# Kernel tuning notes

Hardware: AMD Instinct MI355X
Metric: run time of the kernel (lower is better)

The kernel has to match this reference:

```python
import jax, jax.numpy as jnp
import numpy as np

N = 50000
E = 800000
IO = 128
HID = 256
KQ = 256
EPS = 1e-5


def setup_inputs() -> dict:
    key = jax.random.key(0)
    ks = jax.random.split(key, 16)
    def w(k, shape, fan_in):
        return jax.random.normal(k, shape, dtype=jnp.float32) / np.sqrt(fan_in)
    x0 = jax.random.normal(ks[0], (N, IO), dtype=jnp.float32)
    edges = jax.random.randint(ks[1], (2, E), 0, N, dtype=jnp.int64)
    return {
        "x0": x0,
        "edges": edges,
        "Wq1": w(ks[2], (IO, KQ), IO), "Wk1": w(ks[3], (IO, KQ), IO),
        "Wv1": w(ks[4], (IO, HID), IO), "Wr1": w(ks[5], (IO, HID), IO),
        "b1": jnp.zeros((HID,), jnp.float32),
        "g1": jnp.ones((HID,), jnp.float32), "be1": jnp.zeros((HID,), jnp.float32),
        "Wq2": w(ks[6], (HID, KQ), HID), "Wk2": w(ks[7], (HID, KQ), HID),
        "Wv2": w(ks[8], (HID, IO), HID), "Wr2": w(ks[9], (HID, IO), HID),
        "b2": jnp.zeros((IO,), jnp.float32),
        "g2": jnp.ones((IO,), jnp.float32), "be2": jnp.zeros((IO,), jnp.float32),
    }


def _transformer_conv(x, src, dst, Wq, Wk, Wv, Wr, b, n):
    # single-head graph transformer conv (PyG TransformerConv style)
    q = x @ Wq                      # [n, kq]
    k = x @ Wk                      # [n, kq]
    v = x @ Wv                      # [n, out]
    scale = 1.0 / np.sqrt(Wq.shape[1])
    logits = jnp.sum(q[dst] * k[src], axis=-1) * scale   # [E]
    m = jax.lax.stop_gradient(jax.ops.segment_max(logits, dst, num_segments=n))
    m = jnp.where(jnp.isfinite(m), m, 0.0)
    e = jnp.exp(logits - m[dst])                          # [E]
    s = jax.ops.segment_sum(e, dst, num_segments=n)       # [n]
    alpha = e / jnp.maximum(s[dst], 1e-16)                # [E]
    agg = jax.ops.segment_sum(alpha[:, None] * v[src], dst, num_segments=n)
    return agg + x @ Wr + b


def _batch_norm(x, gamma, beta):
    mu = jnp.mean(x, axis=0)
    var = jnp.mean((x - mu) ** 2, axis=0)  # biased var, as torch BN training
    return (x - mu) * jax.lax.rsqrt(var + EPS) * gamma + beta


def reference(x0, edges, Wq1, Wk1, Wv1, Wr1, b1, g1, be1,
              Wq2, Wk2, Wv2, Wr2, b2, g2, be2):
    src, dst = edges[0], edges[1]
    n = x0.shape[0]
    x = _transformer_conv(x0, src, dst, Wq1, Wk1, Wv1, Wr1, b1, n)
    x = jax.nn.relu(_batch_norm(x, g1, be1))
    x = _transformer_conv(x, src, dst, Wq2, Wk2, Wv2, Wr2, b2, n)
    x = _batch_norm(x, g2, be2)
    return jax.nn.relu(x + x0)
```

## Files before the change

kernel.cpp:

```cpp
#include <hip/hip_runtime.h>
#include <stdint.h>

typedef unsigned short ushort_t;

__device__ __forceinline__ float bf2f(unsigned short u) {
  union { unsigned int i; float f; } c; c.i = ((unsigned int)u) << 16; return c.f;
}
__device__ __forceinline__ unsigned short f2bf(float f) {
  union { float f; unsigned int i; } c; c.f = f;
  unsigned int r = c.i + 0x7FFFu + ((c.i >> 16) & 1u);
  return (unsigned short)(r >> 16);
}
__device__ __forceinline__ float relu_nanprop(float v) { return (v < 0.f) ? 0.f : v; }

__device__ __forceinline__ void async_copy16(const void* g, void* l) {
  __builtin_amdgcn_global_load_lds(
      (const __attribute__((address_space(1))) unsigned int*)(uintptr_t)g,
      (__attribute__((address_space(3))) unsigned int*)(uintptr_t)l,
      16, 0, 0);
}

typedef __attribute__((ext_vector_type(8))) short s16x8;
typedef __attribute__((ext_vector_type(4))) float f32x4;

__device__ __forceinline__ int edge_at(const void* edges, int wide, int idx) {
  if (wide) return (int)((const long long*)edges)[idx];
  return ((const int*)edges)[idx];
}

__global__ void setup_kernel(int* __restrict__ zreg2, int N,
                             const int* __restrict__ e32, int n32, int* __restrict__ eflag,
                             const unsigned int* __restrict__ x, int nw, int* __restrict__ fF) {
  int b = blockIdx.x, tid = threadIdx.x;
  if (b < 256) {
    int total = 2 * N + 1024;
    for (int i = b * 256 + tid; i < total; i += 256 * 256) zreg2[i] = 0;
  } else if (b == 256) {
    __shared__ int any;
    if (tid == 0) any = 0;
    __syncthreads();
    for (int i = tid; i < 4096; i += 256) {
      int idx = 2 * i + 1;
      if (idx < n32 && e32[idx] != 0) any = 1;
    }
    __syncthreads();
    if (tid == 0) eflag[0] = (any == 0) ? 1 : 0;
  } else {
    __shared__ int cnt;
    if (tid == 0) cnt = 0;
    __syncthreads();
    int local = 0;
    for (int i = tid; i < 4096 && i < nw; i += 256) {
      unsigned int low = x[i] & 0xFFFFu;
      unsigned int e = (low >> 7) & 0xFFu;
      if (low != 0u && (e < 96u || e > 144u)) local++;
    }
    atomicAdd(&cnt, local);
    __syncthreads();
    if (tid == 0) fF[0] = (cnt > 1024) ? 1 : 0;
  }
}

__global__ void cvt_all_kernel(const void* __restrict__ x0, ushort_t* __restrict__ x0b, int nx,
                               const void* p0, const void* p1, const void* p2,
                               const void* p3, const void* p4, const void* p5,
                               ushort_t* o0, ushort_t* o1, ushort_t* o2,
                               ushort_t* o3, ushort_t* o4, ushort_t* o5,
                               const void* W10, const void* W11, const void* W12, const void* W13,
                               ushort_t* __restrict__ Wq1b, ushort_t* __restrict__ Wk1b,
                               ushort_t* __restrict__ wcatH1,
                               const void* W20, const void* W21, const void* W22, const void* W23,
                               ushort_t* __restrict__ Wq2b, ushort_t* __restrict__ Wk2b,
                               ushort_t* __restrict__ wcatH2,
                               const void* __restrict__ edges, int* __restrict__ deg,
                               int E, int Nn,
                               const int* __restrict__ eflag, const int* __restrict__ fF) {
  int b = blockIdx.x, tid = threadIdx.x;
  int f = fF[0];
  if (b < 4096) {
    if (f) {
      int nx8 = nx >> 3;
      for (int i = b * 256 + tid; i < nx8; i += 4096 * 256) {
        const float* src = (const float*)x0 + (size_t)i * 8;
        float4 a = *(const float4*)src;
        float4 c = *(const float4*)(src + 4);
        s16x8 r;
        r[0] = (short)f2bf(a.x); r[1] = (short)f2bf(a.y);
        r[2] = (short)f2bf(a.z); r[3] = (short)f2bf(a.w);
        r[4] = (short)f2bf(c.x); r[5] = (short)f2bf(c.y);
        r[6] = (short)f2bf(c.z); r[7] = (short)f2bf(c.w);
        *(s16x8*)(x0b + (size_t)i * 8) = r;
      }
    }
  } else if (b == 4096) {
    const void* ins[6] = {p0, p1, p2, p3, p4, p5};
    ushort_t* outs[6] = {o0, o1, o2, o3, o4, o5};
    const int segs[7] = {0, 256, 512, 768, 896, 1024, 1152};
    for (int i = tid; i < 1152; i += 256) {
      int s = 0;
      while (i >= segs[s + 1]) s++;
      int li = i - segs[s];
      outs[s][li] = f ? f2bf(((const float*)ins[s])[li]) : ((const ushort_t*)ins[s])[li];
    }
  } else if (b < 4609) {
    for (int i = (b - 4097) * 256 + tid; i < 131072; i += 512 * 256) {
      if (i < 32768) {
        Wq1b[i] = f ? f2bf(((const float*)W10)[i]) : ((const ushort_t*)W10)[i];
      } else if (i < 65536) {
        int r = i - 32768;
        Wk1b[r] = f ? f2bf(((const float*)W11)[r]) : ((const ushort_t*)W11)[r];
      } else if (i < 98304) {
        int rem = i - 65536, k = rem >> 8, c = rem & 255;
        ushort_t v = f ? f2bf(((const float*)W13)[rem]) : ((const ushort_t*)W13)[rem];
        wcatH1[(size_t)c * 256 + k] = v;
      } else {
        int rem = i - 98304, k = rem >> 8, c = rem & 255;
        ushort_t v = f ? f2bf(((const float*)W12)[rem]) : ((const ushort_t*)W12)[rem];
        wcatH1[(size_t)c * 256 + 128 + k] = v;
      }
    }
  } else if (b < 5121) {
    for (int i = (b - 4609) * 256 + tid; i < 196608; i += 512 * 256) {
      if (i < 65536) {
        Wq2b[i] = f ? f2bf(((const float*)W20)[i]) : ((const ushort_t*)W20)[i];
      } else if (i < 131072) {
        int r = i - 65536;
        Wk2b[r] = f ? f2bf(((const float*)W21)[r]) : ((const ushort_t*)W21)[r];
      } else if (i < 163840) {
        int rem = i - 131072, k = rem >> 7, c = rem & 127;
        ushort_t v = f ? f2bf(((const float*)W23)[rem]) : ((const ushort_t*)W23)[rem];
        wcatH2[(size_t)c * 512 + k] = v;
      } else {
        int rem = i - 163840, k = rem >> 7, c = rem & 127;
        ushort_t v = f ? f2bf(((const float*)W22)[rem]) : ((const ushort_t*)W22)[rem];
        wcatH2[(size_t)c * 512 + 256 + k] = v;
      }
    }
  } else {
    int wide = eflag[0];
    for (int e = (b - 5121) * 256 + tid; e < E; e += 1024 * 256) {
      int d = edge_at(edges, wide, E + e);
      if (d < 0) d = 0; if (d >= Nn) d = Nn - 1;
      atomicAdd(&deg[d], 1);
    }
  }
}

__global__ void chunk_sum_kernel(const int* __restrict__ deg, int* __restrict__ csum, int n) {
  int b = blockIdx.x, t = threadIdx.x, i = b * 256 + t;
  int v = (i < n) ? deg[i] : 0;
  __shared__ int ws[4];
#pragma unroll
  for (int o = 32; o > 0; o >>= 1) v += __shfl_down(v, o);
  if ((t & 63) == 0) ws[t >> 6] = v;
  __syncthreads();
  if (t == 0) csum[b] = ws[0] + ws[1] + ws[2] + ws[3];
}

__global__ void scan_small_kernel(const int* __restrict__ csum, int* __restrict__ cpre,
                                  int nc, int* __restrict__ offs, int N) {
  __shared__ int tmp[256];
  int t = threadIdx.x;
  int v = (t < nc) ? csum[t] : 0;
  tmp[t] = v;
  __syncthreads();
  for (int off = 1; off < 256; off <<= 1) {
    int x = (t >= off) ? tmp[t - off] : 0;
    __syncthreads();
    tmp[t] += x;
    __syncthreads();
  }
  if (t < nc) cpre[t] = tmp[t] - v;
  if (t == 255) offs[N] = tmp[255];
}

__global__ void scan_final_kernel(const int* __restrict__ deg, const int* __restrict__ cpre,
                                  int* __restrict__ offs, int n) {
  int b = blockIdx.x, t = threadIdx.x, i = b * 256 + t;
  __shared__ int tmp[256];
  int v = (i < n) ? deg[i] : 0;
  tmp[t] = v;
  __syncthreads();
  for (int off = 1; off < 256; off <<= 1) {
    int x = (t >= off) ? tmp[t - off] : 0;
    __syncthreads();
    tmp[t] += x;
    __syncthreads();
  }
  if (i < n) offs[i] = cpre[b] + tmp[t] - v;
}

__global__ void scatter_kernel(const void* __restrict__ edges, const int* __restrict__ flag,
                               const int* __restrict__ offs, int* __restrict__ fill,
                               int* __restrict__ srcS, int E, int Nn) {
  int wide = flag[0];
  for (int e = blockIdx.x * blockDim.x + threadIdx.x; e < E; e += gridDim.x * blockDim.x) {
    int s = edge_at(edges, wide, e);
    int d = edge_at(edges, wide, E + e);
    if (d < 0) d = 0; if (d >= Nn) d = Nn - 1;
    if (s < 0) s = 0; if (s >= Nn) s = Nn - 1;
    int p = offs[d] + atomicAdd(&fill[d], 1);
    if (p < 0) p = 0; if (p >= E) p = E - 1;
    srcS[p] = s;
  }
}

__global__ __launch_bounds__(256)
void mgemm_kernel(const ushort_t* __restrict__ Wk1b, const ushort_t* __restrict__ Wq1b,
                  ushort_t* __restrict__ wcatQ1,
                  const ushort_t* __restrict__ Wk2b, const ushort_t* __restrict__ Wq2b,
                  ushort_t* __restrict__ wcatQ2) {
  __shared__ __align__(16) ushort_t As[128 * 32];
  __shared__ __align__(16) ushort_t Bs[128 * 32];
  const ushort_t* A; const ushort_t* BT; ushort_t* O; int tm, tn, w;
  int b = blockIdx.x;
  if (b == 0) { A = Wk1b; BT = Wq1b; O = wcatQ1; tm = 0; tn = 0; w = 128; }
  else {
    A = Wk2b; BT = Wq2b; O = wcatQ2;
    tm = ((b - 1) >> 1) * 128; tn = ((b - 1) & 1) * 128; w = 256;
  }
  int tid = threadIdx.x;
  int lane = tid & 63, wave = tid >> 6;
  int wm = (wave >> 1) * 64, wn = (wave & 1) * 64;
  int q = lane >> 4, l = lane & 15;
  f32x4 acc[4][4];
#pragma unroll
  for (int a = 0; a < 4; a++)
#pragma unroll
    for (int c = 0; c < 4; c++) acc[a][c] = (f32x4){0.f, 0.f, 0.f, 0.f};
  int lrow = lane >> 2, c8 = (lane & 3) * 8;
  for (int k0 = 0; k0 < 256; k0 += 32) {
#pragma unroll
    for (int t = 0; t < 2; t++) {
      int chunk = t * 4 + wave;
      int row = chunk * 16 + lrow;
      async_copy16(&A[(size_t)(tm + row) * 256 + k0 + c8], &As[chunk * 512]);
      async_copy16(&BT[(size_t)(tn + row) * 256 + k0 + c8], &Bs[chunk * 512]);
    }
    __syncthreads();
    s16x8 af[4], bfr[4];
#pragma unroll
    for (int mf = 0; mf < 4; mf++) af[mf] = *(const s16x8*)&As[(wm + mf * 16 + l) * 32 + q * 8];
#pragma unroll
    for (int nf = 0; nf < 4; nf++) bfr[nf] = *(const s16x8*)&Bs[(wn + nf * 16 + l) * 32 + q * 8];
#pragma unroll
    for (int mf = 0; mf < 4; mf++)
#pragma unroll
      for (int nf = 0; nf < 4; nf++)
        acc[mf][nf] = __builtin_amdgcn_mfma_f32_16x16x32_bf16(af[mf], bfr[nf], acc[mf][nf], 0, 0, 0);
    __syncthreads();
  }
  int lc0 = tn + wn + l;
#pragma unroll
  for (int mf = 0; mf < 4; mf++)
#pragma unroll
    for (int j = 0; j < 4; j++) {
      int r = tm + wm + mf * 16 + q * 4 + j;
#pragma unroll
      for (int nf = 0; nf < 4; nf++)
        O[(size_t)r * w + lc0 + nf * 16] = f2bf(acc[mf][nf][j]);
    }
}

__global__ __launch_bounds__(256)
void gemm4_kernel(const ushort_t* __restrict__ A, const ushort_t* __restrict__ A2,
                  int Ksplit,
                  const ushort_t* __restrict__ BT,
                  ushort_t* __restrict__ o0, ushort_t* __restrict__ o1,
                  ushort_t* __restrict__ o2, ushort_t* __restrict__ o3,
                  const ushort_t* __restrict__ bias3,
                  int M, int K, int NC, int b0, int b1, int b2,
                  float* __restrict__ bnsum, float* __restrict__ bnsq,
                  const int* __restrict__ fF, const void* __restrict__ x0raw, int axsel) {
  __shared__ __align__(16) ushort_t As[128 * 32];
  __shared__ __align__(16) ushort_t Bs[128 * 32];
  const ushort_t* Ae = A;
  const ushort_t* A2e = A2;
  if (axsel && fF[0] == 0) {
    if (axsel & 1) Ae = (const ushort_t*)x0raw;
    if (axsel & 2) A2e = (const ushort_t*)x0raw;
  }
  int tid = threadIdx.x;
  int lane = tid & 63, wave = tid >> 6;
  int tm = blockIdx.x * 128, tn = blockIdx.y * 128;
  int wm = (wave >> 1) * 64, wn = (wave & 1) * 64;
  int q = lane >> 4, l = lane & 15;
  f32x4 acc[4][4];
#pragma unroll
  for (int a = 0; a < 4; a++)
#pragma unroll
    for (int b = 0; b < 4; b++) acc[a][b] = (f32x4){0.f, 0.f, 0.f, 0.f};

  int lrow = lane >> 2, c8 = (lane & 3) * 8;
  for (int k0 = 0; k0 < K; k0 += 32) {
    const ushort_t* Ap; int kk, sA;
    if (k0 < Ksplit) { Ap = Ae;  kk = k0;          sA = Ksplit; }
    else             { Ap = A2e; kk = k0 - Ksplit; sA = K - Ksplit; }
#pragma unroll
    for (int t = 0; t < 2; t++) {
      int chunk = t * 4 + wave;
      int row = chunk * 16 + lrow;
      int ra = tm + row; if (ra > M - 1) ra = M - 1;
      async_copy16(&Ap[(size_t)ra * sA + kk + c8], &As[chunk * 512]);
      async_copy16(&BT[(size_t)(tn + row) * K + k0 + c8], &Bs[chunk * 512]);
    }
    __syncthreads();
    s16x8 af[4], bfr[4];
#pragma unroll
    for (int mf = 0; mf < 4; mf++) af[mf] = *(const s16x8*)&As[(wm + mf * 16 + l) * 32 + q * 8];
#pragma unroll
    for (int nf = 0; nf < 4; nf++) bfr[nf] = *(const s16x8*)&Bs[(wn + nf * 16 + l) * 32 + q * 8];
#pragma unroll
    for (int mf = 0; mf < 4; mf++)
#pragma unroll
      for (int nf = 0; nf < 4; nf++)
        acc[mf][nf] = __builtin_amdgcn_mfma_f32_16x16x32_bf16(af[mf], bfr[nf], acc[mf][nf], 0, 0, 0);
    __syncthreads();
  }
  ushort_t* op; int sbase, w; bool addb = false;
  if (tn < b0)      { op = o0; sbase = 0;  w = b0; }
  else if (tn < b1) { op = o1; sbase = b0; w = b1 - b0; }
  else if (tn < b2) { op = o2; sbase = b1; w = b2 - b1; }
  else              { op = o3; sbase = b2; w = NC - b2; addb = true; }
  int lc0 = tn + wn - sbase + l;
  float bv[4];
#pragma unroll
  for (int nf = 0; nf < 4; nf++) bv[nf] = addb ? bf2f(bias3[lc0 + nf * 16]) : 0.f;
  float csum[4] = {0.f, 0.f, 0.f, 0.f}, csq[4] = {0.f, 0.f, 0.f, 0.f};
#pragma unroll
  for (int mf = 0; mf < 4; mf++) {
#pragma unroll
    for (int j = 0; j < 4; j++) {
      int r = tm + wm + mf * 16 + q * 4 + j;
      if (r < M) {
#pragma unroll
        for (int nf = 0; nf < 4; nf++) {
          float v = acc[mf][nf][j] + bv[nf];
          op[(size_t)r * w + lc0 + nf * 16] = f2bf(v);
          csum[nf] += v;
          csq[nf]  += v * v;
        }
      }
    }
  }
  if (bnsum) {
#pragma unroll
    for (int nf = 0; nf < 4; nf++) {
      csum[nf] += __shfl_xor(csum[nf], 16); csum[nf] += __shfl_xor(csum[nf], 32);
      csq[nf]  += __shfl_xor(csq[nf], 16);  csq[nf]  += __shfl_xor(csq[nf], 32);
    }
    if (q == 0) {
#pragma unroll
      for (int nf = 0; nf < 4; nf++) {
        atomicAdd(&bnsum[lc0 + nf * 16], csum[nf]);
        atomicAdd(&bnsq[lc0 + nf * 16],  csq[nf]);
      }
    }
  }
}

__global__ __launch_bounds__(256)
void attn_kernel(const ushort_t* __restrict__ qt, const ushort_t* __restrict__ xin,
                 const int* __restrict__ offs, const int* __restrict__ srcS,
                 ushort_t* __restrict__ aggb, int D, int Nn,
                 const int* __restrict__ fF, const void* __restrict__ x0raw, int xsel) {
  int lane = threadIdx.x & 63, wave = threadIdx.x >> 6;
  int n = blockIdx.x * 4 + wave;
  if (n >= Nn) return;
  const ushort_t* x = (xsel && fF[0] == 0) ? (const ushort_t*)x0raw : xin;

  int e0 = offs[n], e1 = offs[n + 1];
  float wsum = 0.f;

  if (D == 128) {
    int g = lane >> 3, sub = lane & 7;
    const ushort_t* qp = qt + (size_t)n * 128 + sub * 16;
    s16x8 q0 = __builtin_nontemporal_load((const s16x8*)qp);
    s16x8 q1 = __builtin_nontemporal_load((const s16x8*)(qp + 8));
    float qf[16];
#pragma unroll
    for (int i = 0; i < 8; i++) {
      qf[i]     = bf2f((unsigned short)q0[i]);
      qf[8 + i] = bf2f((unsigned short)q1[i]);
    }
    float acc[16];
#pragma unroll
    for (int i = 0; i < 16; i++) acc[i] = 0.f;
    int j = e0;
    s16x8 x0c, x1c;
    bool have = (j + 8 <= e1);
    if (have) {
      int s = __builtin_nontemporal_load(srcS + j + g);
      if (s < 0 || s >= Nn) s = 0;
      const ushort_t* xp = x + (size_t)s * 128 + sub * 16;
      x0c = *(const s16x8*)xp; x1c = *(const s16x8*)(xp + 8);
    }
    for (; j + 16 <= e1; j += 8) {
      int s2 = __builtin_nontemporal_load(srcS + j + 8 + g);
      if (s2 < 0 || s2 >= Nn) s2 = 0;
      const ushort_t* xp2 = x + (size_t)s2 * 128 + sub * 16;
      s16x8 x0n = *(const s16x8*)xp2, x1n = *(const s16x8*)(xp2 + 8);
      float pa = 0.f, pb = 0.f;
#pragma unroll
      for (int i = 0; i < 8; i++) {
        pa += qf[i] * bf2f((unsigned short)x0c[i]);
        pb += qf[8 + i] * bf2f((unsigned short)x1c[i]);
      }
      float p = pa + pb;
      p += __shfl_xor(p, 1); p += __shfl_xor(p, 2); p += __shfl_xor(p, 4);
      float w = __expf(p * 0.0625f);
      wsum += w;
#pragma unroll
      for (int i = 0; i < 8; i++) {
        acc[i]     += w * bf2f((unsigned short)x0c[i]);
        acc[8 + i] += w * bf2f((unsigned short)x1c[i]);
      }
      x0c = x0n; x1c = x1n;
    }
    if (have) {
      float pa = 0.f, pb = 0.f;
#pragma unroll
      for (int i = 0; i < 8; i++) {
        pa += qf[i] * bf2f((unsigned short)x0c[i]);
        pb += qf[8 + i] * bf2f((unsigned short)x1c[i]);
      }
      float p = pa + pb;
      p += __shfl_xor(p, 1); p += __shfl_xor(p, 2); p += __shfl_xor(p, 4);
      float w = __expf(p * 0.0625f);
      wsum += w;
#pragma unroll
      for (int i = 0; i < 8; i++) {
        acc[i]     += w * bf2f((unsigned short)x0c[i]);
        acc[8 + i] += w * bf2f((unsigned short)x1c[i]);
      }
      j += 8;
    }
    int rem = e1 - j;
    if (rem > 0) {
      bool valid = g < rem;
      int s = __builtin_nontemporal_load(srcS + (valid ? (j + g) : j));
      if (s < 0 || s >= Nn) s = 0;
      const ushort_t* xp = x + (size_t)s * 128 + sub * 16;
      s16x8 x0v = *(const s16x8*)xp, x1v = *(const s16x8*)(xp + 8);
      float pa = 0.f, pb = 0.f;
#pragma unroll
      for (int i = 0; i < 8; i++) {
        pa += qf[i] * bf2f((unsigned short)x0v[i]);
        pb += qf[8 + i] * bf2f((unsigned short)x1v[i]);
      }
      float p = pa + pb;
      p += __shfl_xor(p, 1); p += __shfl_xor(p, 2); p += __shfl_xor(p, 4);
      float w = 0.f;
      if (valid) w = __expf(p * 0.0625f);
      wsum += w;
#pragma unroll
      for (int i = 0; i < 8; i++) {
        acc[i]     += w * bf2f((unsigned short)x0v[i]);
        acc[8 + i] += w * bf2f((unsigned short)x1v[i]);
      }
    }
    wsum += __shfl_xor(wsum, 8); wsum += __shfl_xor(wsum, 16); wsum += __shfl_xor(wsum, 32);
#pragma unroll
    for (int i = 0; i < 16; i++) {
      acc[i] += __shfl_xor(acc[i], 8);
      acc[i] += __shfl_xor(acc[i], 16);
      acc[i] += __shfl_xor(acc[i], 32);
    }
    float inv = 1.f / fmaxf(wsum, 1e-16f);
    if (g == 0) {
      s16x8 r0, r1;
#pragma unroll
      for (int i = 0; i < 8; i++) {
        r0[i] = (short)f2bf(acc[i] * inv);
        r1[i] = (short)f2bf(acc[8 + i] * inv);
      }
      size_t idx = (size_t)n * 128 + sub * 16;
      __builtin_nontemporal_store(r0, (s16x8*)(aggb + idx));
      __builtin_nontemporal_store(r1, (s16x8*)(aggb + idx + 8));
    }
  } else {
    int g = lane >> 4, sub = lane & 15;
    s16x8 q0 = __builtin_nontemporal_load((const s16x8*)(qt + (size_t)n * 256 + sub * 16));
    s16x8 q1 = __builtin_nontemporal_load((const s16x8*)(qt + (size_t)n * 256 + sub * 16 + 8));
    float qf[16];
#pragma unroll
    for (int i = 0; i < 8; i++) {
      qf[i]     = bf2f((unsigned short)q0[i]);
      qf[8 + i] = bf2f((unsigned short)q1[i]);
    }
    float acc[16];
#pragma unroll
    for (int i = 0; i < 16; i++) acc[i] = 0.f;
    int j = e0;
    s16x8 x0c, x1c;
    bool have = (j + 4 <= e1);
    if (have) {
      int s = __builtin_nontemporal_load(srcS + j + g);
      if (s < 0 || s >= Nn) s = 0;
      const ushort_t* xp = x + (size_t)s * 256 + sub * 16;
      x0c = *(const s16x8*)xp; x1c = *(const s16x8*)(xp + 8);
    }
    for (; j + 8 <= e1; j += 4) {
      int s2 = __builtin_nontemporal_load(srcS + j + 4 + g);
      if (s2 < 0 || s2 >= Nn) s2 = 0;
      const ushort_t* xp2 = x + (size_t)s2 * 256 + sub * 16;
      s16x8 x0n = *(const s16x8*)xp2, x1n = *(const s16x8*)(xp2 + 8);
      float pa = 0.f, pb = 0.f;
#pragma unroll
      for (int i = 0; i < 8; i++) {
        pa += qf[i] * bf2f((unsigned short)x0c[i]);
        pb += qf[8 + i] * bf2f((unsigned short)x1c[i]);
      }
      float p = pa + pb;
      p += __shfl_xor(p, 1); p += __shfl_xor(p, 2);
      p += __shfl_xor(p, 4); p += __shfl_xor(p, 8);
      float w = __expf(p * 0.0625f);
      wsum += w;
#pragma unroll
      for (int i = 0; i < 8; i++) {
        acc[i]     += w * bf2f((unsigned short)x0c[i]);
        acc[8 + i] += w * bf2f((unsigned short)x1c[i]);
      }
      x0c = x0n; x1c = x1n;
    }
    if (have) {
      float pa = 0.f, pb = 0.f;
#pragma unroll
      for (int i = 0; i < 8; i++) {
        pa += qf[i] * bf2f((unsigned short)x0c[i]);
        pb += qf[8 + i] * bf2f((unsigned short)x1c[i]);
      }
      float p = pa + pb;
      p += __shfl_xor(p, 1); p += __shfl_xor(p, 2);
      p += __shfl_xor(p, 4); p += __shfl_xor(p, 8);
      float w = __expf(p * 0.0625f);
      wsum += w;
#pragma unroll
      for (int i = 0; i < 8; i++) {
        acc[i]     += w * bf2f((unsigned short)x0c[i]);
        acc[8 + i] += w * bf2f((unsigned short)x1c[i]);
      }
      j += 4;
    }
    int rem = e1 - j;
    if (rem > 0) {
      bool valid = g < rem;
      int s = __builtin_nontemporal_load(srcS + (valid ? (j + g) : j));
      if (s < 0 || s >= Nn) s = 0;
      const ushort_t* xp = x + (size_t)s * 256 + sub * 16;
      s16x8 x0v = *(const s16x8*)xp, x1v = *(const s16x8*)(xp + 8);
      float pa = 0.f, pb = 0.f;
#pragma unroll
      for (int i = 0; i < 8; i++) {
        pa += qf[i] * bf2f((unsigned short)x0v[i]);
        pb += qf[8 + i] * bf2f((unsigned short)x1v[i]);
      }
      float p = pa + pb;
      p += __shfl_xor(p, 1); p += __shfl_xor(p, 2);
      p += __shfl_xor(p, 4); p += __shfl_xor(p, 8);
      float w = 0.f;
      if (valid) w = __expf(p * 0.0625f);
      wsum += w;
#pragma unroll
      for (int i = 0; i < 8; i++) {
        acc[i]     += w * bf2f((unsigned short)x0v[i]);
        acc[8 + i] += w * bf2f((unsigned short)x1v[i]);
      }
    }
    wsum += __shfl_xor(wsum, 16); wsum += __shfl_xor(wsum, 32);
#pragma unroll
    for (int i = 0; i < 16; i++) {
      acc[i] += __shfl_xor(acc[i], 16);
      acc[i] += __shfl_xor(acc[i], 32);
    }
    float inv = 1.f / fmaxf(wsum, 1e-16f);
    if (g == 0) {
      s16x8 r0, r1;
#pragma unroll
      for (int i = 0; i < 8; i++) {
        r0[i] = (short)f2bf(acc[i] * inv);
        r1[i] = (short)f2bf(acc[8 + i] * inv);
      }
      size_t idx = (size_t)n * 256 + sub * 16;
      __builtin_nontemporal_store(r0, (s16x8*)(aggb + idx));
      __builtin_nontemporal_store(r1, (s16x8*)(aggb + idx + 8));
    }
  }
}

__global__ void norm_relu_kernel(const ushort_t* __restrict__ h,
                                 const float* __restrict__ sum, const float* __restrict__ sumsq,
                                 const ushort_t* __restrict__ g, const ushort_t* __restrict__ be,
                                 ushort_t* __restrict__ x1, int N, size_t total8, int cmask) {
  __shared__ float sc[256], sh[256];
  int t = threadIdx.x;
  if (t <= cmask) {
    float mu = sum[t] / (float)N;
    float var = sumsq[t] / (float)N - mu * mu;
    float s = bf2f(g[t]) * rsqrtf(var + 1e-5f);
    sc[t] = s;
    sh[t] = bf2f(be[t]) - mu * s;
  }
  __syncthreads();
  for (size_t i = blockIdx.x * (size_t)blockDim.x + t; i < total8;
       i += (size_t)gridDim.x * blockDim.x) {
    size_t base = i * 8;
    s16x8 hv = *(const s16x8*)(h + base);
    int c0 = (int)(base & (size_t)cmask);
    s16x8 r;
#pragma unroll
    for (int j = 0; j < 8; j++) {
      float vv = bf2f((unsigned short)hv[j]) * sc[c0 + j] + sh[c0 + j];
      r[j] = (short)f2bf(relu_nanprop(vv));
    }
    *(s16x8*)(x1 + base) = r;
  }
}

__global__ void final_kernel(const ushort_t* __restrict__ h,
                             const float* __restrict__ sum, const float* __restrict__ sumsq,
                             const ushort_t* __restrict__ g, const ushort_t* __restrict__ be,
                             const ushort_t* __restrict__ x0b, const void* __restrict__ x0raw,
                             void* __restrict__ out,
                             const int* __restrict__ flagF, int N, size_t total8) {
  __shared__ float sc[128], sh[128];
  int t = threadIdx.x;
  if (t < 128) {
    float mu = sum[t] / (float)N;
    float var = sumsq[t] / (float)N - mu * mu;
    float s = bf2f(g[t]) * rsqrtf(var + 1e-5f);
    sc[t] = s;
    sh[t] = bf2f(be[t]) - mu * s;
  }
  __syncthreads();
  int f = flagF[0];
  const ushort_t* xp = f ? x0b : (const ushort_t*)x0raw;
  for (size_t i = blockIdx.x * (size_t)blockDim.x + t; i < total8;
       i += (size_t)gridDim.x * blockDim.x) {
    size_t base = i * 8;
    s16x8 hv = *(const s16x8*)(h + base);
    s16x8 xv = *(const s16x8*)(xp + base);
    int c0 = (int)(base & 127);
    float v[8];
#pragma unroll
    for (int j = 0; j < 8; j++) {
      float vv = bf2f((unsigned short)hv[j]) * sc[c0 + j] + sh[c0 + j]
               + bf2f((unsigned short)xv[j]);
      v[j] = relu_nanprop(vv);
    }
    if (f) {
      float4 o1 = {v[0], v[1], v[2], v[3]};
      float4 o2 = {v[4], v[5], v[6], v[7]};
      *(float4*)((float*)out + base) = o1;
      *(float4*)((float*)out + base + 4) = o2;
    } else {
      s16x8 r;
#pragma unroll
      for (int j = 0; j < 8; j++) r[j] = (short)f2bf(v[j]);
      *(s16x8*)((ushort_t*)out + base) = r;
    }
  }
}

extern "C" void kernel_launch(void* const* d_in, const int* in_sizes, int n_in,
                              void* d_out, int out_size, void* d_ws, size_t ws_size,
                              hipStream_t stream) {
  const void* x0  = d_in[0];
  const void* edges = d_in[1];
  const void* Wq1 = d_in[2];
  const void* Wk1 = d_in[3];
  const void* Wv1 = d_in[4];
  const void* Wr1 = d_in[5];
  const void* b1  = d_in[6];
  const void* gw1 = d_in[7];
  const void* bw1 = d_in[8];
  const void* Wq2 = d_in[9];
  const void* Wk2 = d_in[10];
  const void* Wv2 = d_in[11];
  const void* Wr2 = d_in[12];
  const void* b2  = d_in[13];
  const void* gw2 = d_in[14];
  const void* bw2 = d_in[15];

  int N = in_sizes[0] / 128;
  int E = in_sizes[1] / 2;
  int NCHUNK = (N + 255) / 256;
  int MT = (N + 127) / 128;

  uintptr_t base = (uintptr_t)d_ws;
  auto carve = [&](size_t bytes) -> void* {
    uintptr_t p = base;
    base += (bytes + 255) & ~(size_t)255;
    return (void*)p;
  };
  ushort_t* x0b = (ushort_t*)carve((size_t)N * 128 * 2);
  ushort_t* qtb = (ushort_t*)carve((size_t)N * 256 * 2);
  ushort_t* aggb = (ushort_t*)carve((size_t)N * 256 * 2);
  ushort_t* hb = (ushort_t*)carve((size_t)N * 256 * 2);
  ushort_t* x1 = (ushort_t*)carve((size_t)N * 256 * 2);
  ushort_t* Wq1b = (ushort_t*)carve((size_t)128 * 256 * 2);
  ushort_t* Wk1b = (ushort_t*)carve((size_t)128 * 256 * 2);
  ushort_t* wcatQ1 = (ushort_t*)carve((size_t)128 * 128 * 2);
  ushort_t* wcatH1 = (ushort_t*)carve((size_t)256 * 256 * 2);
  ushort_t* Wq2b = (ushort_t*)carve((size_t)256 * 256 * 2);
  ushort_t* Wk2b = (ushort_t*)carve((size_t)256 * 256 * 2);
  ushort_t* wcatQ2 = (ushort_t*)carve((size_t)256 * 256 * 2);
  ushort_t* wcatH2 = (ushort_t*)carve((size_t)128 * 512 * 2);
  ushort_t* b1b  = (ushort_t*)carve(256 * 2);
  ushort_t* g1b  = (ushort_t*)carve(256 * 2);
  ushort_t* be1b = (ushort_t*)carve(256 * 2);
  ushort_t* b2b  = (ushort_t*)carve(128 * 2);
  ushort_t* g2b  = (ushort_t*)carve(128 * 2);
  ushort_t* be2b = (ushort_t*)carve(128 * 2);
  int* offs = (int*)carve((size_t)(N + 1) * 4);
  int* srcS = (int*)carve((size_t)E * 4);
  int* csum = (int*)carve(256 * 4);
  int* cpre = (int*)carve(256 * 4);
  int nzero = 2 * N + 1024;
  int* zreg2 = (int*)carve((size_t)nzero * 4);
  int* deg   = zreg2;
  int* fill  = zreg2 + N;
  float* sum1 = (float*)(zreg2 + 2 * N);
  float* sq1  = sum1 + 256;
  float* sum2 = sum1 + 512;
  float* sq2  = sum1 + 640;
  int* eflag = (int*)carve(256);
  int* fF = eflag + 1;

  size_t needed = base - (uintptr_t)d_ws;
  if (needed > ws_size) return;

  setup_kernel<<<258, 256, 0, stream>>>(zreg2, N, (const int*)edges, 2 * E, eflag,
                                        (const unsigned int*)x0, N * 128, fF);
  cvt_all_kernel<<<6145, 256, 0, stream>>>(x0, x0b, N * 128,
                                           b1, gw1, bw1, b2, gw2, bw2,
                                           b1b, g1b, be1b, b2b, g2b, be2b,
                                           Wq1, Wk1, Wv1, Wr1, Wq1b, Wk1b, wcatH1,
                                           Wq2, Wk2, Wv2, Wr2, Wq2b, Wk2b, wcatH2,
                                           edges, deg, E, N, eflag, fF);
  chunk_sum_kernel<<<NCHUNK, 256, 0, stream>>>(deg, csum, N);
  scan_small_kernel<<<1, 256, 0, stream>>>(csum, cpre, NCHUNK, offs, N);
  scan_final_kernel<<<NCHUNK, 256, 0, stream>>>(deg, cpre, offs, N);
  scatter_kernel<<<1024, 256, 0, stream>>>(edges, eflag, offs, fill, srcS, E, N);

  mgemm_kernel<<<5, 256, 0, stream>>>(Wk1b, Wq1b, wcatQ1, Wk2b, Wq2b, wcatQ2);

  int gAttn = (N + 3) / 4;
  gemm4_kernel<<<dim3(MT, 1), 256, 0, stream>>>(x0b, x0b, 128, wcatQ1,
                                                qtb, qtb, qtb, qtb,
                                                b1b, N, 128, 128, 128, 128, 128,
                                                nullptr, nullptr, fF, x0, 3);
  attn_kernel<<<gAttn, 256, 0, stream>>>(qtb, x0b, offs, srcS, aggb, 128, N, fF, x0, 1);
  gemm4_kernel<<<dim3(MT, 2), 256, 0, stream>>>(x0b, aggb, 128, wcatH1,
                                                hb, hb, hb, hb,
                                                b1b, N, 256, 256, 0, 0, 0,
                                                sum1, sq1, fF, x0, 1);
  norm_relu_kernel<<<4096, 256, 0, stream>>>(hb, sum1, sq1, g1b, be1b, x1, N,
                                             (size_t)N * 32, 255);
  gemm4_kernel<<<dim3(MT, 2), 256, 0, stream>>>(x1, x1, 256, wcatQ2,
                                                qtb, qtb, qtb, qtb,
                                                b2b, N, 256, 256, 256, 256, 256,
                                                nullptr, nullptr, fF, x0, 0);
  attn_kernel<<<gAttn, 256, 0, stream>>>(qtb, x1, offs, srcS, aggb, 256, N, fF, x0, 0);
  gemm4_kernel<<<dim3(MT, 1), 256, 0, stream>>>(x1, aggb, 256, wcatH2,
                                                hb, hb, hb, hb,
                                                b2b, N, 512, 128, 0, 0, 0,
                                                sum2, sq2, fF, x0, 0);
  final_kernel<<<2048, 256, 0, stream>>>(hb, sum2, sq2, g2b, be2b, x0b, x0, d_out, fF, N,
                                         (size_t)N * 16);
}
```

Measured before the change: 455.8 us.

## Fuse degree scan with weight GEMM and scatter with first Q projection GEMM

Merges the chunk-sum and small-scan kernels into one launch using a last-block-done counter. The same launch also runs the weight-product GEMM tiles in extra blocks. The CSR scatter kernel and the first-layer query GEMM are placed in one launch so the independent work overlaps. This removes several kernel launches and idle tails, at the cost of an extra atomic counter and a refactored shared gemm_tile helper.

```diff
diff --git a/kernel.cpp b/kernel.cpp
--- a/kernel.cpp
+++ b/kernel.cpp
@@ -28,12 +28,101 @@
   return ((const int*)edges)[idx];
 }
 
+__device__ __forceinline__ void gemm_tile(
+    const ushort_t* __restrict__ Ae, const ushort_t* __restrict__ A2e, int Ksplit,
+    const ushort_t* __restrict__ BT,
+    ushort_t* __restrict__ o0, ushort_t* __restrict__ o1,
+    ushort_t* __restrict__ o2, ushort_t* __restrict__ o3,
+    const ushort_t* __restrict__ bias3,
+    int M, int K, int NC, int b0, int b1, int b2,
+    float* __restrict__ bnsum, float* __restrict__ bnsq,
+    int tm, int tn) {
+  __shared__ __align__(16) ushort_t As[128 * 32];
+  __shared__ __align__(16) ushort_t Bs[128 * 32];
+  int tid = threadIdx.x;
+  int lane = tid & 63, wave = tid >> 6;
+  int wm = (wave >> 1) * 64, wn = (wave & 1) * 64;
+  int q = lane >> 4, l = lane & 15;
+  f32x4 acc[4][4];
+#pragma unroll
+  for (int a = 0; a < 4; a++)
+#pragma unroll
+    for (int b = 0; b < 4; b++) acc[a][b] = (f32x4){0.f, 0.f, 0.f, 0.f};
+
+  int lrow = lane >> 2, c8 = (lane & 3) * 8;
+  for (int k0 = 0; k0 < K; k0 += 32) {
+    const ushort_t* Ap; int kk, sA;
+    if (k0 < Ksplit) { Ap = Ae;  kk = k0;          sA = Ksplit; }
+    else             { Ap = A2e; kk = k0 - Ksplit; sA = K - Ksplit; }
+#pragma unroll
+    for (int t = 0; t < 2; t++) {
+      int chunk = t * 4 + wave;
+      int row = chunk * 16 + lrow;
+      int ra = tm + row; if (ra > M - 1) ra = M - 1;
+      async_copy16(&Ap[(size_t)ra * sA + kk + c8], &As[chunk * 512]);
+      async_copy16(&BT[(size_t)(tn + row) * K + k0 + c8], &Bs[chunk * 512]);
+    }
+    __syncthreads();
+    s16x8 af[4], bfr[4];
+#pragma unroll
+    for (int mf = 0; mf < 4; mf++) af[mf] = *(const s16x8*)&As[(wm + mf * 16 + l) * 32 + q * 8];
+#pragma unroll
+    for (int nf = 0; nf < 4; nf++) bfr[nf] = *(const s16x8*)&Bs[(wn + nf * 16 + l) * 32 + q * 8];
+#pragma unroll
+    for (int mf = 0; mf < 4; mf++)
+#pragma unroll
+      for (int nf = 0; nf < 4; nf++)
+        acc[mf][nf] = __builtin_amdgcn_mfma_f32_16x16x32_bf16(af[mf], bfr[nf], acc[mf][nf], 0, 0, 0);
+    __syncthreads();
+  }
+  ushort_t* op; int sbase, w; bool addb = false;
+  if (tn < b0)      { op = o0; sbase = 0;  w = b0; }
+  else if (tn < b1) { op = o1; sbase = b0; w = b1 - b0; }
+  else if (tn < b2) { op = o2; sbase = b1; w = b2 - b1; }
+  else              { op = o3; sbase = b2; w = NC - b2; addb = true; }
+  int lc0 = tn + wn - sbase + l;
+  float bv[4];
+#pragma unroll
+  for (int nf = 0; nf < 4; nf++) bv[nf] = addb ? bf2f(bias3[lc0 + nf * 16]) : 0.f;
+  float csum[4] = {0.f, 0.f, 0.f, 0.f}, csq[4] = {0.f, 0.f, 0.f, 0.f};
+#pragma unroll
+  for (int mf = 0; mf < 4; mf++) {
+#pragma unroll
+    for (int j = 0; j < 4; j++) {
+      int r = tm + wm + mf * 16 + q * 4 + j;
+      if (r < M) {
+#pragma unroll
+        for (int nf = 0; nf < 4; nf++) {
+          float v = acc[mf][nf][j] + bv[nf];
+          op[(size_t)r * w + lc0 + nf * 16] = f2bf(v);
+          csum[nf] += v;
+          csq[nf]  += v * v;
+        }
+      }
+    }
+  }
+  if (bnsum) {
+#pragma unroll
+    for (int nf = 0; nf < 4; nf++) {
+      csum[nf] += __shfl_xor(csum[nf], 16); csum[nf] += __shfl_xor(csum[nf], 32);
+      csq[nf]  += __shfl_xor(csq[nf], 16);  csq[nf]  += __shfl_xor(csq[nf], 32);
+    }
+    if (q == 0) {
+#pragma unroll
+      for (int nf = 0; nf < 4; nf++) {
+        atomicAdd(&bnsum[lc0 + nf * 16], csum[nf]);
+        atomicAdd(&bnsq[lc0 + nf * 16],  csq[nf]);
+      }
+    }
+  }
+}
+
 __global__ void setup_kernel(int* __restrict__ zreg2, int N,
                              const int* __restrict__ e32, int n32, int* __restrict__ eflag,
                              const unsigned int* __restrict__ x, int nw, int* __restrict__ fF) {
   int b = blockIdx.x, tid = threadIdx.x;
   if (b < 256) {
-    int total = 2 * N + 1024;
+    int total = 2 * N + 1088;
     for (int i = b * 256 + tid; i < total; i += 256 * 256) zreg2[i] = 0;
   } else if (b == 256) {
     __shared__ int any;
@@ -146,32 +235,54 @@
   }
 }
 
-__global__ void chunk_sum_kernel(const int* __restrict__ deg, int* __restrict__ csum, int n) {
-  int b = blockIdx.x, t = threadIdx.x, i = b * 256 + t;
-  int v = (i < n) ? deg[i] : 0;
-  __shared__ int ws[4];
-#pragma unroll
-  for (int o = 32; o > 0; o >>= 1) v += __shfl_down(v, o);
-  if ((t & 63) == 0) ws[t >> 6] = v;
-  __syncthreads();
-  if (t == 0) csum[b] = ws[0] + ws[1] + ws[2] + ws[3];
-}
-
-__global__ void scan_small_kernel(const int* __restrict__ csum, int* __restrict__ cpre,
-                                  int nc, int* __restrict__ offs, int N) {
-  __shared__ int tmp[256];
-  int t = threadIdx.x;
-  int v = (t < nc) ? csum[t] : 0;
-  tmp[t] = v;
-  __syncthreads();
-  for (int off = 1; off < 256; off <<= 1) {
-    int x = (t >= off) ? tmp[t - off] : 0;
-    __syncthreads();
-    tmp[t] += x;
-    __syncthreads();
-  }
-  if (t < nc) cpre[t] = tmp[t] - v;
-  if (t == 255) offs[N] = tmp[255];
+__global__ __launch_bounds__(256)
+void chunk_mgemm_kernel(const int* __restrict__ deg, int* __restrict__ csum,
+                        int* __restrict__ cpre, int* __restrict__ offs,
+                        int n, int N, int nchunk, int* __restrict__ done,
+                        const ushort_t* __restrict__ Wk1b, const ushort_t* __restrict__ Wq1b,
+                        ushort_t* __restrict__ wcatQ1,
+                        const ushort_t* __restrict__ Wk2b, const ushort_t* __restrict__ Wq2b,
+                        ushort_t* __restrict__ wcatQ2) {
+  int b = blockIdx.x, t = threadIdx.x;
+  if (b < nchunk) {
+    int i = b * 256 + t;
+    int v = (i < n) ? deg[i] : 0;
+    __shared__ int ws[4];
+#pragma unroll
+    for (int o = 32; o > 0; o >>= 1) v += __shfl_down(v, o);
+    if ((t & 63) == 0) ws[t >> 6] = v;
+    __syncthreads();
+    if (t == 0) atomicExch(&csum[b], ws[0] + ws[1] + ws[2] + ws[3]);
+    __shared__ int lastf;
+    if (t == 0) lastf = (atomicAdd(done, 1) == nchunk - 1);
+    __syncthreads();
+    if (lastf) {
+      __shared__ int tmp[256];
+      int v2 = (t < nchunk) ? atomicAdd(&csum[t], 0) : 0;
+      tmp[t] = v2;
+      __syncthreads();
+      for (int off = 1; off < 256; off <<= 1) {
+        int x = (t >= off) ? tmp[t - off] : 0;
+        __syncthreads();
+        tmp[t] += x;
+        __syncthreads();
+      }
+      if (t < nchunk) cpre[t] = tmp[t] - v2;
+      if (t == 255) offs[N] = tmp[255];
+    }
+  } else {
+    int mb = b - nchunk;
+    if (mb == 0)
+      gemm_tile(Wk1b, Wk1b, 256, Wq1b, wcatQ1, wcatQ1, wcatQ1, wcatQ1,
+                wcatQ1 , 128, 256, 128, 128, 128, 128,
+                nullptr, nullptr, 0, 0);
+    else {
+      int t2 = mb - 1;
+      gemm_tile(Wk2b, Wk2b, 256, Wq2b, wcatQ2, wcatQ2, wcatQ2, wcatQ2,
+                wcatQ2 , 256, 256, 256, 256, 256, 256,
+                nullptr, nullptr, (t2 >> 1) * 128, (t2 & 1) * 128);
+    }
+  }
 }
 
 __global__ void scan_final_kernel(const int* __restrict__ deg, const int* __restrict__ cpre,
@@ -190,76 +301,30 @@
   if (i < n) offs[i] = cpre[b] + tmp[t] - v;
 }
 
-__global__ void scatter_kernel(const void* __restrict__ edges, const int* __restrict__ flag,
-                               const int* __restrict__ offs, int* __restrict__ fill,
-                               int* __restrict__ srcS, int E, int Nn) {
-  int wide = flag[0];
-  for (int e = blockIdx.x * blockDim.x + threadIdx.x; e < E; e += gridDim.x * blockDim.x) {
-    int s = edge_at(edges, wide, e);
-    int d = edge_at(edges, wide, E + e);
-    if (d < 0) d = 0; if (d >= Nn) d = Nn - 1;
-    if (s < 0) s = 0; if (s >= Nn) s = Nn - 1;
-    int p = offs[d] + atomicAdd(&fill[d], 1);
-    if (p < 0) p = 0; if (p >= E) p = E - 1;
-    srcS[p] = s;
-  }
-}
-
 __global__ __launch_bounds__(256)
-void mgemm_kernel(const ushort_t* __restrict__ Wk1b, const ushort_t* __restrict__ Wq1b,
-                  ushort_t* __restrict__ wcatQ1,
-                  const ushort_t* __restrict__ Wk2b, const ushort_t* __restrict__ Wq2b,
-                  ushort_t* __restrict__ wcatQ2) {
-  __shared__ __align__(16) ushort_t As[128 * 32];
-  __shared__ __align__(16) ushort_t Bs[128 * 32];
-  const ushort_t* A; const ushort_t* BT; ushort_t* O; int tm, tn, w;
+void scatter_qt1_kernel(const void* __restrict__ edges, const int* __restrict__ flag,
+                        const int* __restrict__ offs, int* __restrict__ fill,
+                        int* __restrict__ srcS, int E, int Nn,
+                        const ushort_t* __restrict__ x0b, const ushort_t* __restrict__ wcatQ1,
+                        ushort_t* __restrict__ qtb,
+                        const int* __restrict__ fF, const void* __restrict__ x0raw) {
   int b = blockIdx.x;
-  if (b == 0) { A = Wk1b; BT = Wq1b; O = wcatQ1; tm = 0; tn = 0; w = 128; }
-  else {
-    A = Wk2b; BT = Wq2b; O = wcatQ2;
-    tm = ((b - 1) >> 1) * 128; tn = ((b - 1) & 1) * 128; w = 256;
-  }
-  int tid = threadIdx.x;
-  int lane = tid & 63, wave = tid >> 6;
-  int wm = (wave >> 1) * 64, wn = (wave & 1) * 64;
-  int q = lane >> 4, l = lane & 15;
-  f32x4 acc[4][4];
-#pragma unroll
-  for (int a = 0; a < 4; a++)
-#pragma unroll
-    for (int c = 0; c < 4; c++) acc[a][c] = (f32x4){0.f, 0.f, 0.f, 0.f};
-  int lrow = lane >> 2, c8 = (lane & 3) * 8;
-  for (int k0 = 0; k0 < 256; k0 += 32) {
-#pragma unroll
-    for (int t = 0; t < 2; t++) {
-      int chunk = t * 4 + wave;
-      int row = chunk * 16 + lrow;
-      async_copy16(&A[(size_t)(tm + row) * 256 + k0 + c8], &As[chunk * 512]);
-      async_copy16(&BT[(size_t)(tn + row) * 256 + k0 + c8], &Bs[chunk * 512]);
-    }
-    __syncthreads();
-    s16x8 af[4], bfr[4];
-#pragma unroll
-    for (int mf = 0; mf < 4; mf++) af[mf] = *(const s16x8*)&As[(wm + mf * 16 + l) * 32 + q * 8];
-#pragma unroll
-    for (int nf = 0; nf < 4; nf++) bfr[nf] = *(const s16x8*)&Bs[(wn + nf * 16 + l) * 32 + q * 8];
-#pragma unroll
-    for (int mf = 0; mf < 4; mf++)
-#pragma unroll
-      for (int nf = 0; nf < 4; nf++)
-        acc[mf][nf] = __builtin_amdgcn_mfma_f32_16x16x32_bf16(af[mf], bfr[nf], acc[mf][nf], 0, 0, 0);
-    __syncthreads();
-  }
-  int lc0 = tn + wn + l;
-#pragma unroll
-  for (int mf = 0; mf < 4; mf++)
-#pragma unroll
-    for (int j = 0; j < 4; j++) {
-      int r = tm + wm + mf * 16 + q * 4 + j;
-#pragma unroll
-      for (int nf = 0; nf < 4; nf++)
-        O[(size_t)r * w + lc0 + nf * 16] = f2bf(acc[mf][nf][j]);
-    }
+  if (b < 1024) {
+    int wide = flag[0];
+    for (int e = b * 256 + threadIdx.x; e < E; e += 1024 * 256) {
+      int s = edge_at(edges, wide, e);
+      int d = edge_at(edges, wide, E + e);
+      if (d < 0) d = 0; if (d >= Nn) d = Nn - 1;
+      if (s < 0) s = 0; if (s >= Nn) s = Nn - 1;
+      int p = offs[d] + atomicAdd(&fill[d], 1);
+      if (p < 0) p = 0; if (p >= E) p = E - 1;
+      srcS[p] = s;
+    }
+  } else {
+    const ushort_t* Ae = (fF[0] == 0) ? (const ushort_t*)x0raw : x0b;
+    gemm_tile(Ae, Ae, 128, wcatQ1, qtb, qtb, qtb, qtb, wcatQ1 ,
+              Nn, 128, 128, 128, 128, 128, nullptr, nullptr, (b - 1024) * 128, 0);
+  }
 }
 
 __global__ __launch_bounds__(256)
@@ -272,91 +337,14 @@
                   int M, int K, int NC, int b0, int b1, int b2,
                   float* __restrict__ bnsum, float* __restrict__ bnsq,
                   const int* __restrict__ fF, const void* __restrict__ x0raw, int axsel) {
-  __shared__ __align__(16) ushort_t As[128 * 32];
-  __shared__ __align__(16) ushort_t Bs[128 * 32];
   const ushort_t* Ae = A;
   const ushort_t* A2e = A2;
   if (axsel && fF[0] == 0) {
     if (axsel & 1) Ae = (const ushort_t*)x0raw;
     if (axsel & 2) A2e = (const ushort_t*)x0raw;
   }
-  int tid = threadIdx.x;
-  int lane = tid & 63, wave = tid >> 6;
-  int tm = blockIdx.x * 128, tn = blockIdx.y * 128;
-  int wm = (wave >> 1) * 64, wn = (wave & 1) * 64;
-  int q = lane >> 4, l = lane & 15;
-  f32x4 acc[4][4];
-#pragma unroll
-  for (int a = 0; a < 4; a++)
-#pragma unroll
-    for (int b = 0; b < 4; b++) acc[a][b] = (f32x4){0.f, 0.f, 0.f, 0.f};
-
-  int lrow = lane >> 2, c8 = (lane & 3) * 8;
-  for (int k0 = 0; k0 < K; k0 += 32) {
-    const ushort_t* Ap; int kk, sA;
-    if (k0 < Ksplit) { Ap = Ae;  kk = k0;          sA = Ksplit; }
-    else             { Ap = A2e; kk = k0 - Ksplit; sA = K - Ksplit; }
-#pragma unroll
-    for (int t = 0; t < 2; t++) {
-      int chunk = t * 4 + wave;
-      int row = chunk * 16 + lrow;
-      int ra = tm + row; if (ra > M - 1) ra = M - 1;
-      async_copy16(&Ap[(size_t)ra * sA + kk + c8], &As[chunk * 512]);
-      async_copy16(&BT[(size_t)(tn + row) * K + k0 + c8], &Bs[chunk * 512]);
-    }
-    __syncthreads();
-    s16x8 af[4], bfr[4];
-#pragma unroll
-    for (int mf = 0; mf < 4; mf++) af[mf] = *(const s16x8*)&As[(wm + mf * 16 + l) * 32 + q * 8];
-#pragma unroll
-    for (int nf = 0; nf < 4; nf++) bfr[nf] = *(const s16x8*)&Bs[(wn + nf * 16 + l) * 32 + q * 8];
-#pragma unroll
-    for (int mf = 0; mf < 4; mf++)
-#pragma unroll
-      for (int nf = 0; nf < 4; nf++)
-        acc[mf][nf] = __builtin_amdgcn_mfma_f32_16x16x32_bf16(af[mf], bfr[nf], acc[mf][nf], 0, 0, 0);
-    __syncthreads();
-  }
-  ushort_t* op; int sbase, w; bool addb = false;
-  if (tn < b0)      { op = o0; sbase = 0;  w = b0; }
-  else if (tn < b1) { op = o1; sbase = b0; w = b1 - b0; }
-  else if (tn < b2) { op = o2; sbase = b1; w = b2 - b1; }
-  else              { op = o3; sbase = b2; w = NC - b2; addb = true; }
-  int lc0 = tn + wn - sbase + l;
-  float bv[4];
-#pragma unroll
-  for (int nf = 0; nf < 4; nf++) bv[nf] = addb ? bf2f(bias3[lc0 + nf * 16]) : 0.f;
-  float csum[4] = {0.f, 0.f, 0.f, 0.f}, csq[4] = {0.f, 0.f, 0.f, 0.f};
-#pragma unroll
-  for (int mf = 0; mf < 4; mf++) {
-#pragma unroll
-    for (int j = 0; j < 4; j++) {
-      int r = tm + wm + mf * 16 + q * 4 + j;
-      if (r < M) {
-#pragma unroll
-        for (int nf = 0; nf < 4; nf++) {
-          float v = acc[mf][nf][j] + bv[nf];
-          op[(size_t)r * w + lc0 + nf * 16] = f2bf(v);
-          csum[nf] += v;
-          csq[nf]  += v * v;
-        }
-      }
-    }
-  }
-  if (bnsum) {
-#pragma unroll
-    for (int nf = 0; nf < 4; nf++) {
-      csum[nf] += __shfl_xor(csum[nf], 16); csum[nf] += __shfl_xor(csum[nf], 32);
-      csq[nf]  += __shfl_xor(csq[nf], 16);  csq[nf]  += __shfl_xor(csq[nf], 32);
-    }
-    if (q == 0) {
-#pragma unroll
-      for (int nf = 0; nf < 4; nf++) {
-        atomicAdd(&bnsum[lc0 + nf * 16], csum[nf]);
-        atomicAdd(&bnsq[lc0 + nf * 16],  csq[nf]);
-      }
-    }
-  }
+  gemm_tile(Ae, A2e, Ksplit, BT, o0, o1, o2, o3, bias3, M, K, NC, b0, b1, b2,
+            bnsum, bnsq, blockIdx.x * 128, blockIdx.y * 128);
 }
 
 __global__ __launch_bounds__(256)
@@ -716,7 +704,7 @@
   int* srcS = (int*)carve((size_t)E * 4);
   int* csum = (int*)carve(256 * 4);
   int* cpre = (int*)carve(256 * 4);
-  int nzero = 2 * N + 1024;
+  int nzero = 2 * N + 1088;
   int* zreg2 = (int*)carve((size_t)nzero * 4);
   int* deg   = zreg2;
   int* fill  = zreg2 + N;
@@ -724,6 +712,7 @@
   float* sq1  = sum1 + 256;
   float* sum2 = sum1 + 512;
   float* sq2  = sum1 + 640;
+  int* done  = zreg2 + 2 * N + 1024;
   int* eflag = (int*)carve(256);
   int* fF = eflag + 1;
 
@@ -738,18 +727,14 @@
                                            Wq1, Wk1, Wv1, Wr1, Wq1b, Wk1b, wcatH1,
                                            Wq2, Wk2, Wv2, Wr2, Wq2b, Wk2b, wcatH2,
                                            edges, deg, E, N, eflag, fF);
-  chunk_sum_kernel<<<NCHUNK, 256, 0, stream>>>(deg, csum, N);
-  scan_small_kernel<<<1, 256, 0, stream>>>(csum, cpre, NCHUNK, offs, N);
+  chunk_mgemm_kernel<<<NCHUNK + 5, 256, 0, stream>>>(deg, csum, cpre, offs, N, N, NCHUNK,
+                                                     done, Wk1b, Wq1b, wcatQ1,
+                                                     Wk2b, Wq2b, wcatQ2);
   scan_final_kernel<<<NCHUNK, 256, 0, stream>>>(deg, cpre, offs, N);
-  scatter_kernel<<<1024, 256, 0, stream>>>(edges, eflag, offs, fill, srcS, E, N);
-
-  mgemm_kernel<<<5, 256, 0, stream>>>(Wk1b, Wq1b, wcatQ1, Wk2b, Wq2b, wcatQ2);
+  scatter_qt1_kernel<<<1024 + MT, 256, 0, stream>>>(edges, eflag, offs, fill, srcS, E, N,
+                                                    x0b, wcatQ1, qtb, fF, x0);
 
   int gAttn = (N + 3) / 4;
-  gemm4_kernel<<<dim3(MT, 1), 256, 0, stream>>>(x0b, x0b, 128, wcatQ1,
-                                                qtb, qtb, qtb, qtb,
-                                                b1b, N, 128, 128, 128, 128, 128,
-                                                nullptr, nullptr, fF, x0, 3);
   attn_kernel<<<gAttn, 256, 0, stream>>>(qtb, x0b, offs, srcS, aggb, 128, N, fF, x0, 1);
   gemm4_kernel<<<dim3(MT, 2), 256, 0, stream>>>(x0b, aggb, 128, wcatH1,
                                                 hb, hb, hb, hb,
```

Result: faster. 441.5 us (-3.1%).
